# Performance work log

Hardware: AMD Instinct MI355X
Metric: run time of the kernel (lower is better)

The kernel has to match this reference:

```python
import jax, jax.numpy as jnp
import numpy as np

B, T, D, M = 4, 4096, 1024, 1024
EPS = 1e-6


def _rms_norm(x, w):
    return x * jax.lax.rsqrt(jnp.mean(x * x, axis=-1, keepdims=True) + EPS) * w


def _linrec(xg, r, h0):
    # h_t = x_t + r_t * h_{t-1}  (SRU-style linear recurrence, sqrll_kernel)
    def step(h, inp):
        xt, rt = inp
        h = xt + rt * h
        return h, h
    _, ys = jax.lax.scan(step, h0, (jnp.swapaxes(xg, 0, 1), jnp.swapaxes(r, 0, 1)))
    return jnp.swapaxes(ys, 0, 1)  # [B,T,M]


def setup_inputs() -> dict:
    key = jax.random.key(0)
    ks = jax.random.split(key, 16)
    s = 0.02
    return {
        "x": jax.random.normal(ks[0], (B, T, D), jnp.float32),
        "mem": jnp.zeros((B, M), jnp.float32),
        "norm_w": jnp.ones((D,), jnp.float32),
        "wr_w": jax.random.normal(ks[1], (M, D), jnp.float32) * s,
        "wr_b": jnp.zeros((M,), jnp.float32),
        "wi_w": jax.random.normal(ks[2], (M, D), jnp.float32) * s,
        "wig_w": jax.random.normal(ks[3], (M, D), jnp.float32) * s,
        "wig_b": jnp.zeros((M,), jnp.float32),
        "wog_w": jax.random.normal(ks[4], (M, D), jnp.float32) * s,
        "wog_b": jnp.zeros((M,), jnp.float32),
        "wo_w": jax.random.normal(ks[5], (D, M), jnp.float32) * s,
        "ffnorm_w": jnp.ones((D,), jnp.float32),
        "ffn_wi_w": jax.random.normal(ks[6], (M, D), jnp.float32) * s,
        "ffn_wg_w": jax.random.normal(ks[7], (M, D), jnp.float32) * s,
        "ffn_wg_b": jnp.zeros((M,), jnp.float32),
        "ffn_wo_w": jax.random.normal(ks[8], (D, M), jnp.float32) * s,
    }


def reference(x, mem, norm_w, wr_w, wr_b, wi_w, wig_w, wig_b, wog_w, wog_b,
              wo_w, ffnorm_w, ffn_wi_w, ffn_wg_w, ffn_wg_b, ffn_wo_w):
    # --- sqrll branch ---
    y = _rms_norm(x, norm_w)                                   # [B,T,D]
    ig = jax.nn.sigmoid(jnp.einsum('btd,md->btm', y, wig_w) + wig_b)
    og = jax.nn.sigmoid(jnp.einsum('btd,md->btm', y, wog_w) + wog_b)
    r = jax.nn.sigmoid(jnp.einsum('btd,md->btm', y, wr_w) + wr_b)
    xg = jnp.einsum('btd,md->btm', y, wi_w) * ig               # gated input
    h = _linrec(xg, r, mem)                                    # [B,T,M]
    mem_out = jax.lax.stop_gradient(h[:, -1])
    s = (h / (1.0 + jnp.abs(h))) * og                          # softsign * out gate
    x = x + jnp.einsum('btm,dm->btd', s, wo_w)                 # residual (dropout=0)
    # --- gated FFN branch ---
    z = _rms_norm(x, ffnorm_w)
    ff = jnp.einsum('btd,md->btm', z, ffn_wi_w) * jax.nn.sigmoid(
        jnp.einsum('btd,md->btm', z, ffn_wg_w) + ffn_wg_b)
    x = x + jnp.einsum('btm,dm->btd', ff, ffn_wo_w)
    return (x, mem_out)
```

## Files before the change

### kernel.cpp

```cpp
#include <hip/hip_runtime.h>
#include <stdint.h>


#define R_ROWS 16384
#define DIM    1024
#define MDIM   1024
#define TSEQ   4096
#define NCHUNK 64
#define TCH    64

typedef __attribute__((ext_vector_type(8))) short  bf16x8;
typedef __attribute__((ext_vector_type(8))) ushort u16x8;
typedef __attribute__((ext_vector_type(4))) float  f32x4;

__device__ __forceinline__ float bf2f(ushort u) {
  union { float f; unsigned int i; } x; x.i = ((unsigned int)u) << 16; return x.f;
}
__device__ __forceinline__ ushort f2bf(float f) {
  union { float f; unsigned int i; } x; x.f = f;
  unsigned int r = x.i + 0x7fffu + ((x.i >> 16) & 1u);
  return (ushort)(r >> 16);
}
__device__ __forceinline__ float sigmoidf_(float x) {
  return 1.0f / (1.0f + __expf(-x));
}
__device__ __forceinline__ void load_lds16(const void* g, void* s) {
  __builtin_amdgcn_global_load_lds(
      (const __attribute__((address_space(1))) void*)g,
      (__attribute__((address_space(3))) void*)s, 16, 0, 0);
}

__global__ __launch_bounds__(256)
void cvt_weights(const float* __restrict__ w0, const float* __restrict__ w1,
                 const float* __restrict__ w2, const float* __restrict__ w3,
                 const float* __restrict__ w4, const float* __restrict__ w5,
                 const float* __restrict__ w6, ushort* __restrict__ dst)
{
  const float* src;
  switch (blockIdx.y) {
    case 0: src = w0; break; case 1: src = w1; break;
    case 2: src = w2; break; case 3: src = w3; break;
    case 4: src = w4; break; case 5: src = w5; break;
    default: src = w6; break;
  }
  const int i = blockIdx.x * 256 + threadIdx.x;
  const size_t off = (size_t)blockIdx.y * 1048576 + (size_t)i * 4;
  const float4 v = *(const float4*)(src + (size_t)i * 4);
  ushort4 o; o.x = f2bf(v.x); o.y = f2bf(v.y); o.z = f2bf(v.z); o.w = f2bf(v.w);
  *(ushort4*)(dst + off) = o;
}

__global__ __launch_bounds__(256)
void cvt_one(const float* __restrict__ src, ushort* __restrict__ dst)
{
  const int i = blockIdx.x * 256 + threadIdx.x;
  const float4 v = *(const float4*)(src + (size_t)i * 4);
  ushort4 o; o.x = f2bf(v.x); o.y = f2bf(v.y); o.z = f2bf(v.z); o.w = f2bf(v.w);
  *(ushort4*)(dst + (size_t)i * 4) = o;
}

template<bool IN_F32>
__global__ __launch_bounds__(256)
void rmsnorm_k(const void* __restrict__ xin, const float* __restrict__ w,
               ushort* __restrict__ y)
{
  __shared__ float red[4];
  const int row = blockIdx.x;
  const int tid = threadIdx.x;
  const size_t base = (size_t)row * DIM + tid * 4;
  float v[4];
  if (IN_F32) {
    const float4 xv = *(const float4*)((const float*)xin + base);
    v[0] = xv.x; v[1] = xv.y; v[2] = xv.z; v[3] = xv.w;
  } else {
    const ushort4 xv = *(const ushort4*)((const ushort*)xin + base);
    v[0] = bf2f(xv.x); v[1] = bf2f(xv.y); v[2] = bf2f(xv.z); v[3] = bf2f(xv.w);
  }
  float ss = v[0]*v[0] + v[1]*v[1] + v[2]*v[2] + v[3]*v[3];
  for (int o = 32; o > 0; o >>= 1) ss += __shfl_down(ss, o, 64);
  const int wave = tid >> 6, lane = tid & 63;
  if (lane == 0) red[wave] = ss;
  __syncthreads();
  const float sum = red[0] + red[1] + red[2] + red[3];
  const float scale = rsqrtf(sum * (1.0f / DIM) + 1e-6f);
  const float4 wv = *(const float4*)(w + tid * 4);
  ushort4 o4;
  o4.x = f2bf(v[0] * scale * wv.x);
  o4.y = f2bf(v[1] * scale * wv.y);
  o4.z = f2bf(v[2] * scale * wv.z);
  o4.w = f2bf(v[3] * scale * wv.w);
  *(ushort4*)(y + base) = o4;
}

template<int MODE>
__global__ __launch_bounds__(512, 2)
void gemm8(const ushort* __restrict__ A, const ushort* __restrict__ W,
           const float* __restrict__ bias, const float* __restrict__ auxf,
           const ushort* __restrict__ auxb, ushort* __restrict__ outb,
           float* __restrict__ outf)
{
  __shared__ __align__(16) ushort lds[2][2][2][8192];
  const int tid  = threadIdx.x;
  const int bm = blockIdx.x, bn = blockIdx.y;
  const int wave = tid >> 6, lane = tid & 63;
  const int wm = wave >> 2, wn = wave & 3;
  const int quad = lane >> 4, l16 = lane & 15;
  const int axor = l16 & 7;

  const ushort* Ab = A + (size_t)bm * (256 * 1024);
  const ushort* Wb = W + (size_t)bn * (256 * 1024);

  f32x4 acc[8][4];
#pragma unroll
  for (int i = 0; i < 8; ++i)
#pragma unroll
    for (int j = 0; j < 4; ++j) acc[i][j] = (f32x4){0.f, 0.f, 0.f, 0.f};

  auto stage = [&](const ushort* __restrict__ base, int kt, int mat, int half) {
    ushort* dst = &lds[kt & 1][mat][half][0];
    const ushort* src = base + (size_t)half * (128 * 1024) + kt * 64;
#pragma unroll
    for (int q = 0; q < 2; ++q) {
      const int ci = q * 512 + tid;
      const int row = ci >> 3, c8 = ci & 7;
      load_lds16(src + (size_t)row * 1024 + ((c8 ^ (row & 7)) << 3),
                 dst + ci * 8);
    }
  };

  stage(Ab, 0, 0, 0); stage(Ab, 0, 0, 1);
  stage(Wb, 0, 1, 0); stage(Wb, 0, 1, 1);
  stage(Wb, 1, 1, 0); stage(Wb, 1, 1, 1);
  asm volatile("s_waitcnt vmcnt(4)" ::: "memory");
  __builtin_amdgcn_s_barrier();

  for (int ktc = 0; ktc < 16; ++ktc) {
    const int b = ktc & 1;
    const ushort* Ah = &lds[b][0][wm][0];
    const ushort* Bh = &lds[b][1][wn >> 1][0];
    const int brow0 = (wn & 1) * 64;
    bf16x8 bfr[4][2];
#pragma unroll
    for (int q = 0; q < 4; ++q) {
      if (q == 0) {
#pragma unroll
        for (int j = 0; j < 4; ++j)
#pragma unroll
          for (int ks = 0; ks < 2; ++ks)
            bfr[j][ks] = *(const bf16x8*)
                &Bh[(brow0 + j * 16 + l16) * 64 +
                    (((ks * 4 + quad) ^ axor) << 3)];
      }
      bf16x8 af[2][2];
#pragma unroll
      for (int p = 0; p < 2; ++p)
#pragma unroll
        for (int ks = 0; ks < 2; ++ks)
          af[p][ks] = *(const bf16x8*)
              &Ah[((2 * q + p) * 16 + l16) * 64 +
                  (((ks * 4 + quad) ^ axor) << 3)];
      if (q == 0 && ktc + 1 < 16) stage(Ab, ktc + 1, 0, 0);
      if (q == 1 && ktc + 1 < 16) stage(Ab, ktc + 1, 0, 1);
      if (q == 2 && ktc + 2 < 16) stage(Wb, ktc + 2, 1, 0);
      if (q == 3 && ktc + 2 < 16) stage(Wb, ktc + 2, 1, 1);
      __builtin_amdgcn_s_barrier();
      asm volatile("s_waitcnt lgkmcnt(0)" ::: "memory");
      __builtin_amdgcn_s_setprio(1);
#pragma unroll
      for (int p = 0; p < 2; ++p)
#pragma unroll
        for (int j = 0; j < 4; ++j)
#pragma unroll
          for (int ks = 0; ks < 2; ++ks)
            acc[2 * q + p][j] = __builtin_amdgcn_mfma_f32_16x16x32_bf16(
                af[p][ks], bfr[j][ks], acc[2 * q + p][j], 0, 0, 0);
      __builtin_amdgcn_s_setprio(0);
      if (q == 3) {
        if (ktc >= 14) asm volatile("s_waitcnt vmcnt(0)" ::: "memory");
        else           asm volatile("s_waitcnt vmcnt(4)" ::: "memory");
      }
      __builtin_amdgcn_s_barrier();
    }
  }

  float* C = (float*)&lds[0][0][0][0];
#pragma unroll 1
  for (int h = 0; h < 2; ++h) {
    if (wm == h) {
      const int cb = wn * 64;
#pragma unroll
      for (int i = 0; i < 8; ++i)
#pragma unroll
        for (int j = 0; j < 4; ++j)
#pragma unroll
          for (int g = 0; g < 4; ++g) {
            const int rw = i * 16 + quad * 4 + g;
            const int cw = cb + j * 16 + l16;
            C[rw * 256 + (cw ^ (((rw >> 2) & 1) << 4))] = acc[i][j][g];
          }
    }
    __syncthreads();
#pragma unroll 1
    for (int sp = 0; sp < 16; ++sp) {
      const int lin = sp * 2048 + tid * 4;
      const int row = lin >> 8, c4 = lin & 255;
      const int xr = ((row >> 2) & 1) << 4;
      const float4 v4 = *(const float4*)&C[row * 256 + (c4 ^ xr)];
      const int rg = bm * 256 + h * 128 + row;
      const int cg = bn * 256 + c4;
      const size_t gidx = (size_t)rg * 1024 + cg;
      if (MODE == 0) {
        const float4 bv = *(const float4*)(bias + cg);
        ushort4 o;
        o.x = f2bf(sigmoidf_(v4.x + bv.x));
        o.y = f2bf(sigmoidf_(v4.y + bv.y));
        o.z = f2bf(sigmoidf_(v4.z + bv.z));
        o.w = f2bf(sigmoidf_(v4.w + bv.w));
        *(ushort4*)(outb + gidx) = o;
      } else if (MODE == 1) {
        const float4 a4 = *(const float4*)(auxf + gidx);
        ushort4 o;
        o.x = f2bf(v4.x + a4.x); o.y = f2bf(v4.y + a4.y);
        o.z = f2bf(v4.z + a4.z); o.w = f2bf(v4.w + a4.w);
        *(ushort4*)(outb + gidx) = o;
      } else if (MODE == 2) {
        const ushort4 a4 = *(const ushort4*)(auxb + gidx);
        ushort4 o;
        o.x = f2bf(v4.x * bf2f(a4.x)); o.y = f2bf(v4.y * bf2f(a4.y));
        o.z = f2bf(v4.z * bf2f(a4.z)); o.w = f2bf(v4.w * bf2f(a4.w));
        *(ushort4*)(outb + gidx) = o;
      } else {
        const ushort4 a4 = *(const ushort4*)(auxb + gidx);
        float4 o;
        o.x = v4.x + bf2f(a4.x); o.y = v4.y + bf2f(a4.y);
        o.z = v4.z + bf2f(a4.z); o.w = v4.w + bf2f(a4.w);
        *(float4*)(outf + gidx) = o;
      }
    }
    __syncthreads();
  }
}

__global__ __launch_bounds__(256)
void linrec_passA(ushort* __restrict__ xg, const ushort* __restrict__ r,
                  float* __restrict__ cL, float* __restrict__ cP)
{
  const int g = blockIdx.x * 256 + threadIdx.x;
  const int m4 = (g & 255) << 2;
  const int bc = g >> 8;
  const int b = bc >> 6, c = bc & 63;
  const size_t base = ((size_t)(b * TSEQ + c * TCH)) * MDIM + m4;
  float h0 = 0.f, h1 = 0.f, h2 = 0.f, h3 = 0.f;
  float p0 = 1.f, p1 = 1.f, p2 = 1.f, p3 = 1.f;
  for (int t = 0; t < TCH; ++t) {
    const size_t idx = base + (size_t)t * MDIM;
    const ushort4 xv = *(const ushort4*)&xg[idx];
    const ushort4 rv = *(const ushort4*)&r[idx];
    const float r0 = bf2f(rv.x), r1 = bf2f(rv.y), r2 = bf2f(rv.z), r3 = bf2f(rv.w);
    h0 = fmaf(r0, h0, bf2f(xv.x)); p0 *= r0;
    h1 = fmaf(r1, h1, bf2f(xv.y)); p1 *= r1;
    h2 = fmaf(r2, h2, bf2f(xv.z)); p2 *= r2;
    h3 = fmaf(r3, h3, bf2f(xv.w)); p3 *= r3;
    ushort4 o; o.x = f2bf(h0); o.y = f2bf(h1); o.z = f2bf(h2); o.w = f2bf(h3);
    *(ushort4*)&xg[idx] = o;
  }
  const size_t cb = (size_t)c * 4096 + b * MDIM + m4;
  float4 L4; L4.x = h0; L4.y = h1; L4.z = h2; L4.w = h3;
  float4 P4; P4.x = p0; P4.y = p1; P4.z = p2; P4.w = p3;
  *(float4*)&cL[cb] = L4;
  *(float4*)&cP[cb] = P4;
}

__global__ __launch_bounds__(256)
void linrec_passB(const float* __restrict__ cL, const float* __restrict__ cP,
                  const float* __restrict__ mem, float* __restrict__ cIn,
                  float* __restrict__ memout)
{
  const int g = blockIdx.x * 256 + threadIdx.x;
  float carry = mem[g];
  for (int c = 0; c < NCHUNK; ++c) {
    cIn[c * 4096 + g] = carry;
    carry = fmaf(cP[c * 4096 + g], carry, cL[c * 4096 + g]);
  }
  memout[g] = carry;
}

__global__ __launch_bounds__(256)
void linrec_passC(const ushort* __restrict__ L, const ushort* __restrict__ r,
                  const ushort* __restrict__ og, const float* __restrict__ cIn,
                  ushort* __restrict__ s)
{
  const int g = blockIdx.x * 256 + threadIdx.x;
  const int m4 = (g & 255) << 2;
  const int bc = g >> 8;
  const int b = bc >> 6, c = bc & 63;
  const size_t base = ((size_t)(b * TSEQ + c * TCH)) * MDIM + m4;
  const size_t cb = (size_t)c * 4096 + b * MDIM + m4;
  const float4 ci = *(const float4*)&cIn[cb];
  float p0 = 1.f, p1 = 1.f, p2 = 1.f, p3 = 1.f;
  for (int t = 0; t < TCH; ++t) {
    const size_t idx = base + (size_t)t * MDIM;
    const ushort4 rv = *(const ushort4*)&r[idx];
    const ushort4 lv = *(const ushort4*)&L[idx];
    const ushort4 ov = *(const ushort4*)&og[idx];
    p0 *= bf2f(rv.x); p1 *= bf2f(rv.y); p2 *= bf2f(rv.z); p3 *= bf2f(rv.w);
    const float a0 = fmaf(p0, ci.x, bf2f(lv.x));
    const float a1 = fmaf(p1, ci.y, bf2f(lv.y));
    const float a2 = fmaf(p2, ci.z, bf2f(lv.z));
    const float a3 = fmaf(p3, ci.w, bf2f(lv.w));
    ushort4 o;
    o.x = f2bf(a0 / (1.0f + fabsf(a0)) * bf2f(ov.x));
    o.y = f2bf(a1 / (1.0f + fabsf(a1)) * bf2f(ov.y));
    o.z = f2bf(a2 / (1.0f + fabsf(a2)) * bf2f(ov.z));
    o.w = f2bf(a3 / (1.0f + fabsf(a3)) * bf2f(ov.w));
    *(ushort4*)&s[idx] = o;
  }
}

extern "C" void kernel_launch(void* const* d_in, const int* in_sizes, int n_in,
                              void* d_out, int out_size, void* d_ws, size_t ws_size,
                              hipStream_t stream)
{
  const float* x        = (const float*)d_in[0];
  const float* mem      = (const float*)d_in[1];
  const float* norm_w   = (const float*)d_in[2];
  const float* wr_w     = (const float*)d_in[3];
  const float* wr_b     = (const float*)d_in[4];
  const float* wi_w     = (const float*)d_in[5];
  const float* wig_w    = (const float*)d_in[6];
  const float* wig_b    = (const float*)d_in[7];
  const float* wog_w    = (const float*)d_in[8];
  const float* wog_b    = (const float*)d_in[9];
  const float* wo_w     = (const float*)d_in[10];
  const float* ffnorm_w = (const float*)d_in[11];
  const float* ffn_wi_w = (const float*)d_in[12];
  const float* ffn_wg_w = (const float*)d_in[13];
  const float* ffn_wg_b = (const float*)d_in[14];
  const float* ffn_wo_w = (const float*)d_in[15];
  float* outF = (float*)d_out;

  ushort* xgL  = (ushort*)d_out;
  ushort* wbf  = (ushort*)((char*)d_out + 33554432ULL);
  float*  memoutF = outF + 16777216;

  char* ws = (char*)d_ws;
  ushort* y   = (ushort*)(ws);
  ushort* r   = (ushort*)(ws + 33554432ULL);
  ushort* og  = (ushort*)(ws + 67108864ULL);
  float*  cL  = (float*) (ws + 100663296ULL);
  float*  cP  = (float*) (ws + 101711872ULL);
  float*  cIn = (float*) (ws + 102760448ULL);
  ushort* s   = y;
  ushort* x1  = og;
  ushort* z   = r;
  ushort* gf  = y;
  ushort* fwo_bf = (ushort*)(ws + 100663296ULL);

  ushort* wr_bf   = wbf + 0 * 1048576;
  ushort* wog_bf  = wbf + 1 * 1048576;
  ushort* wi_bf   = wbf + 2 * 1048576;
  ushort* wig_bf  = wbf + 3 * 1048576;
  ushort* wo_bf   = wbf + 4 * 1048576;
  ushort* fwi_bf  = wbf + 5 * 1048576;
  ushort* fwg_bf  = wbf + 6 * 1048576;

  const dim3 g8(64, 4);

  cvt_weights<<<dim3(1024, 7), 256, 0, stream>>>(
      wr_w, wog_w, wi_w, wig_w, wo_w, ffn_wi_w, ffn_wg_w, wbf);

  rmsnorm_k<true><<<R_ROWS, 256, 0, stream>>>(x, norm_w, y);
  gemm8<0><<<g8, 512, 0, stream>>>(y, wr_bf,  wr_b,  nullptr, nullptr, r,   nullptr);
  gemm8<0><<<g8, 512, 0, stream>>>(y, wog_bf, wog_b, nullptr, nullptr, og,  nullptr);
  gemm8<0><<<g8, 512, 0, stream>>>(y, wig_bf, wig_b, nullptr, nullptr, xgL, nullptr);
  gemm8<2><<<g8, 512, 0, stream>>>(y, wi_bf,  nullptr, nullptr, xgL, xgL, nullptr);
  linrec_passA<<<256, 256, 0, stream>>>(xgL, r, cL, cP);
  linrec_passB<<<16, 256, 0, stream>>>(cL, cP, mem, cIn, memoutF);
  linrec_passC<<<256, 256, 0, stream>>>(xgL, r, og, cIn, s);
  cvt_one<<<1024, 256, 0, stream>>>(ffn_wo_w, fwo_bf);
  gemm8<1><<<g8, 512, 0, stream>>>(s, wo_bf, nullptr, x, nullptr, x1, nullptr);
  rmsnorm_k<false><<<R_ROWS, 256, 0, stream>>>(x1, ffnorm_w, z);
  gemm8<0><<<g8, 512, 0, stream>>>(z, fwg_bf, ffn_wg_b, nullptr, nullptr, gf, nullptr);
  gemm8<2><<<g8, 512, 0, stream>>>(z, fwi_bf, nullptr, nullptr, gf, gf, nullptr);
  gemm8<3><<<g8, 512, 0, stream>>>(gf, fwo_bf, nullptr, nullptr, x1, nullptr, outF);
}
```

Baseline: 569.5 us.

## Batch three sigmoid-gate GEMMs into one launch, halve scan chunk, widen epilogue stores

The wr, wog and wig projections now run as a single GEMM launch over a 64x12 grid. The weights are laid out contiguously and each column group picks its own bias and output buffer, which cuts launch count and tail effects. The linear-recurrence chunk length drops from 64 to 32 with twice as many chunks, giving passA and passC more parallelism at the cost of a longer serial carry pass. The GEMM epilogue now writes 8-wide vectors, staging addresses are precomputed, and the trailing barrier is dropped. Chunk buffers move into spare output memory, and the ffn_wo conversion is moved earlier in the launch order.

```diff
diff --git a/kernel.cpp b/kernel.cpp
--- a/kernel.cpp
+++ b/kernel.cpp
@@ -6,8 +6,8 @@
 #define DIM    1024
 #define MDIM   1024
 #define TSEQ   4096
-#define NCHUNK 64
-#define TCH    64
+#define NCHUNK 128
+#define TCH    32
 
 typedef __attribute__((ext_vector_type(8))) short  bf16x8;
 typedef __attribute__((ext_vector_type(8))) ushort u16x8;
@@ -97,7 +97,9 @@
 void gemm8(const ushort* __restrict__ A, const ushort* __restrict__ W,
            const float* __restrict__ bias, const float* __restrict__ auxf,
            const ushort* __restrict__ auxb, ushort* __restrict__ outb,
-           float* __restrict__ outf)
+           float* __restrict__ outf,
+           const float* __restrict__ bias2, const float* __restrict__ bias3,
+           ushort* __restrict__ outb2, ushort* __restrict__ outb3)
 {
   __shared__ __align__(16) ushort lds[2][2][2][8192];
   const int tid  = threadIdx.x;
@@ -116,21 +118,17 @@
 #pragma unroll
     for (int j = 0; j < 4; ++j) acc[i][j] = (f32x4){0.f, 0.f, 0.f, 0.f};
 
-  auto stage = [&](const ushort* __restrict__ base, int kt, int mat, int half) {
-    ushort* dst = &lds[kt & 1][mat][half][0];
-    const ushort* src = base + (size_t)half * (128 * 1024) + kt * 64;
-#pragma unroll
-    for (int q = 0; q < 2; ++q) {
-      const int ci = q * 512 + tid;
-      const int row = ci >> 3, c8 = ci & 7;
-      load_lds16(src + (size_t)row * 1024 + ((c8 ^ (row & 7)) << 3),
-                 dst + ci * 8);
-    }
+  const int ci0 = tid, ci1 = tid + 512;
+  const size_t gs0 = (size_t)(ci0 >> 3) * 1024 + (size_t)((((ci0 & 7) ^ ((ci0 >> 3) & 7))) << 3);
+  const size_t gs1 = (size_t)(ci1 >> 3) * 1024 + (size_t)((((ci1 & 7) ^ ((ci1 >> 3) & 7))) << 3);
+  auto stage = [&](const ushort* __restrict__ src, ushort* dst) {
+    load_lds16(src + gs0, dst + ci0 * 8);
+    load_lds16(src + gs1, dst + ci1 * 8);
   };
 
-  stage(Ab, 0, 0, 0); stage(Ab, 0, 0, 1);
-  stage(Wb, 0, 1, 0); stage(Wb, 0, 1, 1);
-  stage(Wb, 1, 1, 0); stage(Wb, 1, 1, 1);
+  stage(Ab,          &lds[0][0][0][0]); stage(Ab + 131072,      &lds[0][0][1][0]);
+  stage(Wb,          &lds[0][1][0][0]); stage(Wb + 131072,      &lds[0][1][1][0]);
+  stage(Wb + 64,     &lds[1][1][0][0]); stage(Wb + 131072 + 64, &lds[1][1][1][0]);
   asm volatile("s_waitcnt vmcnt(4)" ::: "memory");
   __builtin_amdgcn_s_barrier();
 
@@ -159,10 +157,14 @@
           af[p][ks] = *(const bf16x8*)
               &Ah[((2 * q + p) * 16 + l16) * 64 +
                   (((ks * 4 + quad) ^ axor) << 3)];
-      if (q == 0 && ktc + 1 < 16) stage(Ab, ktc + 1, 0, 0);
-      if (q == 1 && ktc + 1 < 16) stage(Ab, ktc + 1, 0, 1);
-      if (q == 2 && ktc + 2 < 16) stage(Wb, ktc + 2, 1, 0);
-      if (q == 3 && ktc + 2 < 16) stage(Wb, ktc + 2, 1, 1);
+      if (q == 0 && ktc + 1 < 16)
+        stage(Ab + (ktc + 1) * 64, &lds[(ktc + 1) & 1][0][0][0]);
+      if (q == 1 && ktc + 1 < 16)
+        stage(Ab + 131072 + (ktc + 1) * 64, &lds[(ktc + 1) & 1][0][1][0]);
+      if (q == 2 && ktc + 2 < 16)
+        stage(Wb + (ktc + 2) * 64, &lds[ktc & 1][1][0][0]);
+      if (q == 3 && ktc + 2 < 16)
+        stage(Wb + 131072 + (ktc + 2) * 64, &lds[ktc & 1][1][1][0]);
       __builtin_amdgcn_s_barrier();
       asm volatile("s_waitcnt lgkmcnt(0)" ::: "memory");
       __builtin_amdgcn_s_setprio(1);
@@ -184,6 +186,15 @@
   }
 
   float* C = (float*)&lds[0][0][0][0];
+  ushort* ob = outb;
+  const float* bp = bias;
+  int colbase = bn * 256;
+  if (MODE == 4) {
+    const int grp = bn >> 2;
+    ob = (grp == 0) ? outb : (grp == 1) ? outb2 : outb3;
+    bp = (grp == 0) ? bias : (grp == 1) ? bias2 : bias3;
+    colbase = (bn & 3) * 256;
+  }
 #pragma unroll 1
   for (int h = 0; h < 2; ++h) {
     if (wm == h) {
@@ -201,43 +212,53 @@
     }
     __syncthreads();
 #pragma unroll 1
-    for (int sp = 0; sp < 16; ++sp) {
-      const int lin = sp * 2048 + tid * 4;
-      const int row = lin >> 8, c4 = lin & 255;
+    for (int sp = 0; sp < 8; ++sp) {
+      const int lin = sp * 4096 + tid * 8;
+      const int row = lin >> 8, c8 = lin & 255;
       const int xr = ((row >> 2) & 1) << 4;
-      const float4 v4 = *(const float4*)&C[row * 256 + (c4 ^ xr)];
+      const int cx = c8 ^ xr;
+      const float4 vA = *(const float4*)&C[row * 256 + cx];
+      const float4 vB = *(const float4*)&C[row * 256 + cx + 4];
       const int rg = bm * 256 + h * 128 + row;
-      const int cg = bn * 256 + c4;
-      const size_t gidx = (size_t)rg * 1024 + cg;
-      if (MODE == 0) {
-        const float4 bv = *(const float4*)(bias + cg);
-        ushort4 o;
-        o.x = f2bf(sigmoidf_(v4.x + bv.x));
-        o.y = f2bf(sigmoidf_(v4.y + bv.y));
-        o.z = f2bf(sigmoidf_(v4.z + bv.z));
-        o.w = f2bf(sigmoidf_(v4.w + bv.w));
-        *(ushort4*)(outb + gidx) = o;
+      const size_t gidx = (size_t)rg * 1024 + colbase + c8;
+      if (MODE == 0 || MODE == 4) {
+        const float4 b0 = *(const float4*)(bp + colbase + c8);
+        const float4 b1 = *(const float4*)(bp + colbase + c8 + 4);
+        u16x8 o;
+        o[0] = f2bf(sigmoidf_(vA.x + b0.x)); o[1] = f2bf(sigmoidf_(vA.y + b0.y));
+        o[2] = f2bf(sigmoidf_(vA.z + b0.z)); o[3] = f2bf(sigmoidf_(vA.w + b0.w));
+        o[4] = f2bf(sigmoidf_(vB.x + b1.x)); o[5] = f2bf(sigmoidf_(vB.y + b1.y));
+        o[6] = f2bf(sigmoidf_(vB.z + b1.z)); o[7] = f2bf(sigmoidf_(vB.w + b1.w));
+        *(u16x8*)(ob + gidx) = o;
       } else if (MODE == 1) {
-        const float4 a4 = *(const float4*)(auxf + gidx);
-        ushort4 o;
-        o.x = f2bf(v4.x + a4.x); o.y = f2bf(v4.y + a4.y);
-        o.z = f2bf(v4.z + a4.z); o.w = f2bf(v4.w + a4.w);
-        *(ushort4*)(outb + gidx) = o;
+        const float4 a0 = *(const float4*)(auxf + gidx);
+        const float4 a1 = *(const float4*)(auxf + gidx + 4);
+        u16x8 o;
+        o[0] = f2bf(vA.x + a0.x); o[1] = f2bf(vA.y + a0.y);
+        o[2] = f2bf(vA.z + a0.z); o[3] = f2bf(vA.w + a0.w);
+        o[4] = f2bf(vB.x + a1.x); o[5] = f2bf(vB.y + a1.y);
+        o[6] = f2bf(vB.z + a1.z); o[7] = f2bf(vB.w + a1.w);
+        *(u16x8*)(ob + gidx) = o;
       } else if (MODE == 2) {
-        const ushort4 a4 = *(const ushort4*)(auxb + gidx);
-        ushort4 o;
-        o.x = f2bf(v4.x * bf2f(a4.x)); o.y = f2bf(v4.y * bf2f(a4.y));
-        o.z = f2bf(v4.z * bf2f(a4.z)); o.w = f2bf(v4.w * bf2f(a4.w));
-        *(ushort4*)(outb + gidx) = o;
+        const u16x8 a8 = *(const u16x8*)(auxb + gidx);
+        u16x8 o;
+        o[0] = f2bf(vA.x * bf2f(a8[0])); o[1] = f2bf(vA.y * bf2f(a8[1]));
+        o[2] = f2bf(vA.z * bf2f(a8[2])); o[3] = f2bf(vA.w * bf2f(a8[3]));
+        o[4] = f2bf(vB.x * bf2f(a8[4])); o[5] = f2bf(vB.y * bf2f(a8[5]));
+        o[6] = f2bf(vB.z * bf2f(a8[6])); o[7] = f2bf(vB.w * bf2f(a8[7]));
+        *(u16x8*)(ob + gidx) = o;
       } else {
-        const ushort4 a4 = *(const ushort4*)(auxb + gidx);
-        float4 o;
-        o.x = v4.x + bf2f(a4.x); o.y = v4.y + bf2f(a4.y);
-        o.z = v4.z + bf2f(a4.z); o.w = v4.w + bf2f(a4.w);
-        *(float4*)(outf + gidx) = o;
+        const u16x8 a8 = *(const u16x8*)(auxb + gidx);
+        float4 o0, o1;
+        o0.x = vA.x + bf2f(a8[0]); o0.y = vA.y + bf2f(a8[1]);
+        o0.z = vA.z + bf2f(a8[2]); o0.w = vA.w + bf2f(a8[3]);
+        o1.x = vB.x + bf2f(a8[4]); o1.y = vB.y + bf2f(a8[5]);
+        o1.z = vB.z + bf2f(a8[6]); o1.w = vB.w + bf2f(a8[7]);
+        *(float4*)(outf + gidx) = o0;
+        *(float4*)(outf + gidx + 4) = o1;
       }
     }
-    __syncthreads();
+    if (h == 0) __syncthreads();
   }
 }
 
@@ -248,7 +269,7 @@
   const int g = blockIdx.x * 256 + threadIdx.x;
   const int m4 = (g & 255) << 2;
   const int bc = g >> 8;
-  const int b = bc >> 6, c = bc & 63;
+  const int b = bc >> 7, c = bc & 127;
   const size_t base = ((size_t)(b * TSEQ + c * TCH)) * MDIM + m4;
   float h0 = 0.f, h1 = 0.f, h2 = 0.f, h3 = 0.f;
   float p0 = 1.f, p1 = 1.f, p2 = 1.f, p3 = 1.f;
@@ -278,6 +299,7 @@
 {
   const int g = blockIdx.x * 256 + threadIdx.x;
   float carry = mem[g];
+#pragma unroll 4
   for (int c = 0; c < NCHUNK; ++c) {
     cIn[c * 4096 + g] = carry;
     carry = fmaf(cP[c * 4096 + g], carry, cL[c * 4096 + g]);
@@ -293,7 +315,7 @@
   const int g = blockIdx.x * 256 + threadIdx.x;
   const int m4 = (g & 255) << 2;
   const int bc = g >> 8;
-  const int b = bc >> 6, c = bc & 63;
+  const int b = bc >> 7, c = bc & 127;
   const size_t base = ((size_t)(b * TSEQ + c * TCH)) * MDIM + m4;
   const size_t cb = (size_t)c * 4096 + b * MDIM + m4;
   const float4 ci = *(const float4*)&cIn[cb];
@@ -341,46 +363,49 @@
 
   ushort* xgL  = (ushort*)d_out;
   ushort* wbf  = (ushort*)((char*)d_out + 33554432ULL);
+  float*  cL   = (float*)((char*)d_out + 48234496ULL);
+  float*  cP   = (float*)((char*)d_out + 50331648ULL);
+  float*  cIn  = (float*)((char*)d_out + 52428800ULL);
   float*  memoutF = outF + 16777216;
 
   char* ws = (char*)d_ws;
   ushort* y   = (ushort*)(ws);
   ushort* r   = (ushort*)(ws + 33554432ULL);
   ushort* og  = (ushort*)(ws + 67108864ULL);
-  float*  cL  = (float*) (ws + 100663296ULL);
-  float*  cP  = (float*) (ws + 101711872ULL);
-  float*  cIn = (float*) (ws + 102760448ULL);
+  ushort* fwo_bf = (ushort*)(ws + 100663296ULL);
   ushort* s   = y;
   ushort* x1  = og;
   ushort* z   = r;
   ushort* gf  = y;
-  ushort* fwo_bf = (ushort*)(ws + 100663296ULL);
 
   ushort* wr_bf   = wbf + 0 * 1048576;
-  ushort* wog_bf  = wbf + 1 * 1048576;
-  ushort* wi_bf   = wbf + 2 * 1048576;
-  ushort* wig_bf  = wbf + 3 * 1048576;
+  ushort* wi_bf   = wbf + 3 * 1048576;
   ushort* wo_bf   = wbf + 4 * 1048576;
   ushort* fwi_bf  = wbf + 5 * 1048576;
   ushort* fwg_bf  = wbf + 6 * 1048576;
 
   const dim3 g8(64, 4);
+  const dim3 g83(64, 12);
 
   cvt_weights<<<dim3(1024, 7), 256, 0, stream>>>(
-      wr_w, wog_w, wi_w, wig_w, wo_w, ffn_wi_w, ffn_wg_w, wbf);
+      wr_w, wog_w, wig_w, wi_w, wo_w, ffn_wi_w, ffn_wg_w, wbf);
+  cvt_one<<<1024, 256, 0, stream>>>(ffn_wo_w, fwo_bf);
 
   rmsnorm_k<true><<<R_ROWS, 256, 0, stream>>>(x, norm_w, y);
-  gemm8<0><<<g8, 512, 0, stream>>>(y, wr_bf,  wr_b,  nullptr, nullptr, r,   nullptr);
-  gemm8<0><<<g8, 512, 0, stream>>>(y, wog_bf, wog_b, nullptr, nullptr, og,  nullptr);
-  gemm8<0><<<g8, 512, 0, stream>>>(y, wig_bf, wig_b, nullptr, nullptr, xgL, nullptr);
-  gemm8<2><<<g8, 512, 0, stream>>>(y, wi_bf,  nullptr, nullptr, xgL, xgL, nullptr);
-  linrec_passA<<<256, 256, 0, stream>>>(xgL, r, cL, cP);
+  gemm8<4><<<g83, 512, 0, stream>>>(y, wr_bf, wr_b, nullptr, nullptr, r, nullptr,
+                                    wog_b, wig_b, og, xgL);
+  gemm8<2><<<g8, 512, 0, stream>>>(y, wi_bf, nullptr, nullptr, xgL, xgL, nullptr,
+                                   nullptr, nullptr, nullptr, nullptr);
+  linrec_passA<<<512, 256, 0, stream>>>(xgL, r, cL, cP);
   linrec_passB<<<16, 256, 0, stream>>>(cL, cP, mem, cIn, memoutF);
-  linrec_passC<<<256, 256, 0, stream>>>(xgL, r, og, cIn, s);
-  cvt_one<<<1024, 256, 0, stream>>>(ffn_wo_w, fwo_bf);
-  gemm8<1><<<g8, 512, 0, stream>>>(s, wo_bf, nullptr, x, nullptr, x1, nullptr);
+  linrec_passC<<<512, 256, 0, stream>>>(xgL, r, og, cIn, s);
+  gemm8<1><<<g8, 512, 0, stream>>>(s, wo_bf, nullptr, x, nullptr, x1, nullptr,
+                                   nullptr, nullptr, nullptr, nullptr);
   rmsnorm_k<false><<<R_ROWS, 256, 0, stream>>>(x1, ffnorm_w, z);
-  gemm8<0><<<g8, 512, 0, stream>>>(z, fwg_bf, ffn_wg_b, nullptr, nullptr, gf, nullptr);
-  gemm8<2><<<g8, 512, 0, stream>>>(z, fwi_bf, nullptr, nullptr, gf, gf, nullptr);
-  gemm8<3><<<g8, 512, 0, stream>>>(gf, fwo_bf, nullptr, nullptr, x1, nullptr, outF);
-}
+  gemm8<0><<<g8, 512, 0, stream>>>(z, fwg_bf, ffn_wg_b, nullptr, nullptr, gf, nullptr,
+                                   nullptr, nullptr, nullptr, nullptr);
+  gemm8<2><<<g8, 512, 0, stream>>>(z, fwi_bf, nullptr, nullptr, gf, gf, nullptr,
+                                   nullptr, nullptr, nullptr, nullptr);
+  gemm8<3><<<g8, 512, 0, stream>>>(gf, fwo_bf, nullptr, nullptr, x1, nullptr, outF,
+                                   nullptr, nullptr, nullptr, nullptr);
+}
```

New measurement: 556.3 us. -2.3%, faster.
